# Optimization experiments

Hardware: AMD Instinct MI355X
Metric: run time of the kernel (lower is better)

Reference implementation:

```python
import jax, jax.numpy as jnp
import numpy as np

# module config (init_kwargs)
AH, AW = 14, 14            # aligned_height, aligned_width
SCALE = 0.25               # spatial_scale
RATIO = 2                  # sampling_ratio
SHIFT = 0.0                # spatial_shift (added in feature-map coords)
HALF_PART = 0              # 0 = full box
ROI_SCALE = 1.0            # box rescale about its center


def setup_inputs() -> dict:
    key = jax.random.key(0)
    kf, kb, kx, ky, kw, kh = jax.random.split(key, 6)
    B, C, H, W = 2, 256, 200, 272
    N = 256
    features = jax.random.normal(kf, (B, C, H, W), dtype=jnp.float32)
    img_h, img_w = H / SCALE, W / SCALE
    bidx = jax.random.randint(kb, (N,), 0, B).astype(jnp.float32)
    x1 = jax.random.uniform(kx, (N,)) * (img_w * 0.6)
    y1 = jax.random.uniform(ky, (N,)) * (img_h * 0.6)
    bw = 32.0 + jax.random.uniform(kw, (N,)) * (img_w * 0.35)
    bh = 32.0 + jax.random.uniform(kh, (N,)) * (img_h * 0.35)
    rois = jnp.stack([bidx, x1, y1, x1 + bw, y1 + bh], axis=1).astype(jnp.float32)
    return {"features": features, "rois": rois}


def _lin_idx(coord, size):
    # bilinear index/weight prep with RoIAlign boundary rules
    valid = (coord > -1.0) & (coord < float(size))
    c = jnp.clip(coord, 0.0, float(size - 1))
    lo = jnp.floor(c)
    hi = jnp.minimum(lo + 1.0, float(size - 1))
    frac = c - lo
    return lo.astype(jnp.int32), hi.astype(jnp.int32), frac, valid.astype(coord.dtype)


def _roi_mask_align(features, rois):
    B, C, H, W = features.shape
    N = rois.shape[0]
    PH, PW, r = AH + 1, AW + 1, RATIO
    b = rois[:, 0].astype(jnp.int32)
    # to feature-map coords, with roi_scale about the box center and spatial_shift
    x1, y1, x2, y2 = (rois[:, 1] * SCALE, rois[:, 2] * SCALE,
                      rois[:, 3] * SCALE, rois[:, 4] * SCALE)
    cx, cy = 0.5 * (x1 + x2), 0.5 * (y1 + y2)
    hw, hh = 0.5 * (x2 - x1) * ROI_SCALE, 0.5 * (y2 - y1) * ROI_SCALE
    x1, x2 = cx - hw + SHIFT, cx + hw + SHIFT
    y1, y2 = cy - hh + SHIFT, cy + hh + SHIFT
    roi_w = jnp.maximum(x2 - x1, 1.0)
    roi_h = jnp.maximum(y2 - y1, 1.0)
    bin_w = roi_w / PW
    bin_h = roi_h / PH
    # sample coords, separable: sx [N, PW*r], sy [N, PH*r]
    ix = jnp.arange(PW * r, dtype=jnp.float32)
    iy = jnp.arange(PH * r, dtype=jnp.float32)
    sx = x1[:, None] + (ix[None, :] + 0.5) * (bin_w[:, None] / r)
    sy = y1[:, None] + (iy[None, :] + 0.5) * (bin_h[:, None] / r)
    y_lo, y_hi, fy, vy = _lin_idx(sy, H)
    x_lo, x_hi, fx, vx = _lin_idx(sx, W)
    featsT = jnp.transpose(features, (0, 2, 3, 1))  # [B,H,W,C]
    bb = b[:, None, None]
    gather = lambda yi, xi: featsT[bb, yi[:, :, None], xi[:, None, :]]  # [N,Sy,Sx,C]
    wy0, wy1 = 1.0 - fy, fy
    wx0, wx1 = 1.0 - fx, fx
    val = (gather(y_lo, x_lo) * (wy0[:, :, None] * wx0[:, None, :])[..., None]
           + gather(y_lo, x_hi) * (wy0[:, :, None] * wx1[:, None, :])[..., None]
           + gather(y_hi, x_lo) * (wy1[:, :, None] * wx0[:, None, :])[..., None]
           + gather(y_hi, x_hi) * (wy1[:, :, None] * wx1[:, None, :])[..., None])
    val = val * (vy[:, :, None] * vx[:, None, :])[..., None]
    # average the r*r samples per bin -> [N, PH, PW, C]
    val = val.reshape(N, PH, r, PW, r, C).mean(axis=(2, 4))
    return jnp.transpose(val, (0, 3, 1, 2))  # [N, C, PH, PW]


def reference(features, rois):
    x = _roi_mask_align(features, rois)  # [N, C, AH+1, AW+1]
    # avg_pool2d(kernel=2, stride=1)
    out = 0.25 * (x[..., :-1, :-1] + x[..., 1:, :-1]
                  + x[..., :-1, 1:] + x[..., 1:, 1:])
    return out  # [N, C, AH, AW]
```

## Files before the change

kernel.cpp:

```cpp
#include <hip/hip_runtime.h>


#define AH_  14
#define AW_  14
#define C_   256
#define H_   200
#define W_   272
#define HW_  (H_ * W_)
#define CPB  4
#define WBUF 2056

#define GLOAD_LDS16(g, l)                                                     \
  __builtin_amdgcn_global_load_lds(                                           \
      (const __attribute__((address_space(1))) void*)(g),                     \
      (__attribute__((address_space(3))) void*)(l), 16, 0, 0)

__global__ __launch_bounds__(128)
void roi_mask_align_avg_kernel(const float* __restrict__ feat,
                               const float* __restrict__ rois,
                               float* __restrict__ out) {
    __shared__ float Ls[2][WBUF];

    const int p   = blockIdx.x;
    const int xcd = p & 7;
    const int q   = p >> 3;
    const int n   = q & 255;
    const int cgi = q >> 8;
    const int cg  = cgi * 8 + xcd;
    const int c0  = cg * CPB;

    const int tid  = threadIdx.x;
    const int wave = tid >> 6;
    const int lane = tid & 63;
    const int half = lane >> 5;
    const int ix   = lane & 31;

    float* __restrict__ LsW = Ls[wave];
    {
        float4* L4 = (float4*)LsW;
        for (int o = lane; o < WBUF / 4; o += 64)
            L4[o] = make_float4(0.f, 0.f, 0.f, 0.f);
    }
    asm volatile("s_waitcnt lgkmcnt(0)" ::: "memory");

    const float r0f = rois[n * 5 + 0];
    const float x1s = rois[n * 5 + 1] * 0.25f;
    const float y1s = rois[n * 5 + 2] * 0.25f;
    const float x2s = rois[n * 5 + 3] * 0.25f;
    const float y2s = rois[n * 5 + 4] * 0.25f;
    const int   b   = (int)r0f;

    const float cx = 0.5f * (x1s + x2s), cy = 0.5f * (y1s + y2s);
    const float hw = 0.5f * (x2s - x1s), hh = 0.5f * (y2s - y1s);
    const float x1 = cx - hw, x2 = cx + hw;
    const float y1 = cy - hh, y2 = cy + hh;
    const float roi_w = fmaxf(x2 - x1, 1.0f);
    const float roi_h = fmaxf(y2 - y1, 1.0f);
    const float sub_w = roi_w * (1.0f / 15.0f) * 0.5f;
    const float sub_h = roi_h * (1.0f / 15.0f) * 0.5f;

    const float sx  = x1 + ((float)ix + 0.5f) * sub_w;
    const bool  vx_ = (sx > -1.0f) && (sx < (float)W_) && (ix < 30);
    const float ccx = fminf(fmaxf(sx, 0.0f), (float)(W_ - 1));
    const float lox = floorf(ccx);
    const int   xl  = (int)lox;
    const int   xh  = min(xl + 1, W_ - 1);
    const float fx  = ccx - lox;
    const float vmx = vx_ ? 1.0f : 0.0f;
    const float wx0 = (1.0f - fx) * vmx;
    const float wx1 = fx * vmx;

    const int s0    = __builtin_amdgcn_readfirstlane(xl);
    const int s0c0  = min(s0, W_ - 128);
    const int s0c1  = max(min(s0 - 8, W_ - 128), 0);
    const int s0ch  = half ? s0c1 : s0c0;
    const int xh29  = __builtin_amdgcn_readlane(xh, 29);
    const int spanh = xh29 - s0ch;
    const bool ldact = (ix * 4) <= spanh;
    const int iA    = half * 128 + (xl - s0ch);

    const float* __restrict__ bpA = feat + ((size_t)b * C_ + c0) * (size_t)HW_;
    const float* __restrict__ gAl = bpA + (size_t)half * HW_ + s0ch + 4 * ix;
    const float* __restrict__ gBl = gAl + 2 * HW_;

    const int  aw   = ix >> 1;
    const bool emit = ((lane & 1) == 0) && (aw < AW_);
    const int  iy0  = wave * 14;

    auto geom = [&](int iy, int& olo, int& ohi, float& wy0, float& wy1) {
        const float sy  = y1 + ((float)iy + 0.5f) * sub_h;
        const bool  vy_ = (sy > -1.0f) && (sy < (float)H_);
        const float ccy = fminf(fmaxf(sy, 0.0f), (float)(H_ - 1));
        const float loy = floorf(ccy);
        const float fy  = ccy - loy;
        const float vmy = vy_ ? 1.0f : 0.0f;
        wy0 = (1.0f - fy) * vmy;
        wy1 = fy * vmy;
        const int yl_s = __builtin_amdgcn_readfirstlane((int)loy);
        const int yh_s = min(yl_s + 1, H_ - 1);
        olo = yl_s * W_;
        ohi = yh_s * W_;
    };
    auto stage = [&](int bb, int olo, int ohi) {
        float* d = LsW + bb * 1024;
        if (ldact) {
            GLOAD_LDS16(gAl + olo, d);
            GLOAD_LDS16(gBl + olo, d + 256);
            GLOAD_LDS16(gAl + ohi, d + 512);
            GLOAD_LDS16(gBl + ohi, d + 768);
        }
    };

    int   olo_c, ohi_c;  float wy0_c, wy1_c;
    geom(iy0, olo_c, ohi_c, wy0_c, wy1_c);
    stage(0, olo_c, ohi_c);

    float outA[7], outB[7];
    float prevSA = 0.f, prevSB = 0.f, PA = 0.f, PB = 0.f;

    #pragma unroll
    for (int i = 0; i < 16; ++i) {
        int olo_n, ohi_n; float wy0_n, wy1_n;
        geom(iy0 + i + 1, olo_n, ohi_n, wy0_n, wy1_n);

        asm volatile("s_waitcnt lgkmcnt(0)" ::: "memory");

        stage((i + 1) & 1, olo_n, ohi_n);

        asm volatile("s_waitcnt vmcnt(4)" ::: "memory");

        const float* d = LsW + (i & 1) * 1024;
        const float alo0 = d[iA],       alo1 = d[iA + 1];
        const float blo0 = d[256 + iA], blo1 = d[256 + iA + 1];
        const float ahi0 = d[512 + iA], ahi1 = d[512 + iA + 1];
        const float bhi0 = d[768 + iA], bhi1 = d[768 + iA + 1];

        const float w00 = wy0_c * wx0, w01 = wy0_c * wx1;
        const float w10 = wy1_c * wx0, w11 = wy1_c * wx1;
        PA += alo0 * w00 + alo1 * w01 + ahi0 * w10 + ahi1 * w11;
        PB += blo0 * w00 + blo1 * w01 + bhi0 * w10 + bhi1 * w11;

        if (i & 1) {
            const float tA = PA + __shfl_xor(PA, 1, 64);
            const float uA = tA + __shfl_down(tA, 2, 64);
            const float tB = PB + __shfl_xor(PB, 1, 64);
            const float uB = tB + __shfl_down(tB, 2, 64);
            const int kk = i >> 1;
            if (kk > 0) {
                outA[kk - 1] = (prevSA + uA) * 0.0625f;
                outB[kk - 1] = (prevSB + uB) * 0.0625f;
            }
            prevSA = uA; prevSB = uB;
            PA = 0.f; PB = 0.f;
        }
        olo_c = olo_n; ohi_c = ohi_n; wy0_c = wy0_n; wy1_c = wy1_n;
    }

    asm volatile("s_waitcnt vmcnt(0)" ::: "memory");
    if (emit) {
        #pragma unroll
        for (int k = 0; k < 7; ++k) {
            LsW[half * 98 + k * AW_ + aw]       = outA[k];
            LsW[(2 + half) * 98 + k * AW_ + aw] = outB[k];
        }
    }

    float* __restrict__ op = out + ((size_t)n * C_ + c0) * (AH_ * AW_);
    for (int o = lane; o < CPB * 7 * AW_; o += 64) {
        const int ch  = o / 98;
        const int rem = o - ch * 98;
        op[ch * (AH_ * AW_) + wave * 98 + rem] = LsW[o];
    }
}

extern "C" void kernel_launch(void* const* d_in, const int* in_sizes, int n_in,
                              void* d_out, int out_size, void* d_ws, size_t ws_size,
                              hipStream_t stream) {
    const float* feat = (const float*)d_in[0];
    const float* rois = (const float*)d_in[1];
    float* out = (float*)d_out;
    const int grid = 256 * (C_ / CPB);
    roi_mask_align_avg_kernel<<<grid, 128, 0, stream>>>(feat, rois, out);
}
```

Baseline: 252.7 us.

## Reuse loaded feature rows across consecutive y samples and drop double buffering

Precomputes per-sample y geometry once per lane and classifies each sample row as a full reuse, a shift (the previous hi row becomes lo), or a new load. Only rows that are actually new get fetched into LDS, which cuts redundant global loads when samples share rows. The LDS zero-init and the double buffer are removed, and the launch bound is raised to 8 blocks for higher occupancy. The trade-off is that each load is now waited on synchronously (vmcnt(0)), so the previous overlap of prefetch with compute is lost.

```diff
diff --git a/kernel.cpp b/kernel.cpp
--- a/kernel.cpp
+++ b/kernel.cpp
@@ -8,18 +8,17 @@
 #define W_   272
 #define HW_  (H_ * W_)
 #define CPB  4
-#define WBUF 2056
 
 #define GLOAD_LDS16(g, l)                                                     \
   __builtin_amdgcn_global_load_lds(                                           \
       (const __attribute__((address_space(1))) void*)(g),                     \
       (__attribute__((address_space(3))) void*)(l), 16, 0, 0)
 
-__global__ __launch_bounds__(128)
+__global__ __launch_bounds__(128, 8)
 void roi_mask_align_avg_kernel(const float* __restrict__ feat,
                                const float* __restrict__ rois,
                                float* __restrict__ out) {
-    __shared__ float Ls[2][WBUF];
+    __shared__ float Ls[2][1024];
 
     const int p   = blockIdx.x;
     const int xcd = p & 7;
@@ -36,12 +35,6 @@
     const int ix   = lane & 31;
 
     float* __restrict__ LsW = Ls[wave];
-    {
-        float4* L4 = (float4*)LsW;
-        for (int o = lane; o < WBUF / 4; o += 64)
-            L4[o] = make_float4(0.f, 0.f, 0.f, 0.f);
-    }
-    asm volatile("s_waitcnt lgkmcnt(0)" ::: "memory");
 
     const float r0f = rois[n * 5 + 0];
     const float x1s = rois[n * 5 + 1] * 0.25f;
@@ -71,72 +64,80 @@
     const float wx1 = fx * vmx;
 
     const int s0    = __builtin_amdgcn_readfirstlane(xl);
-    const int s0c0  = min(s0, W_ - 128);
-    const int s0c1  = max(min(s0 - 8, W_ - 128), 0);
-    const int s0ch  = half ? s0c1 : s0c0;
+    const int s0c   = min(s0, W_ - 128);
     const int xh29  = __builtin_amdgcn_readlane(xh, 29);
-    const int spanh = xh29 - s0ch;
+    const int spanh = xh29 - s0c;
     const bool ldact = (ix * 4) <= spanh;
-    const int iA    = half * 128 + (xl - s0ch);
+    const int iA    = half * 128 + (vx_ ? (xl - s0c) : 0);
 
     const float* __restrict__ bpA = feat + ((size_t)b * C_ + c0) * (size_t)HW_;
-    const float* __restrict__ gAl = bpA + (size_t)half * HW_ + s0ch + 4 * ix;
+    const float* __restrict__ gAl = bpA + (size_t)half * HW_ + s0c + 4 * ix;
     const float* __restrict__ gBl = gAl + 2 * HW_;
 
     const int  aw   = ix >> 1;
     const bool emit = ((lane & 1) == 0) && (aw < AW_);
     const int  iy0  = wave * 14;
 
-    auto geom = [&](int iy, int& olo, int& ohi, float& wy0, float& wy1) {
-        const float sy  = y1 + ((float)iy + 0.5f) * sub_h;
-        const bool  vy_ = (sy > -1.0f) && (sy < (float)H_);
-        const float ccy = fminf(fmaxf(sy, 0.0f), (float)(H_ - 1));
-        const float loy = floorf(ccy);
-        const float fy  = ccy - loy;
-        const float vmy = vy_ ? 1.0f : 0.0f;
-        wy0 = (1.0f - fy) * vmy;
-        wy1 = fy * vmy;
-        const int yl_s = __builtin_amdgcn_readfirstlane((int)loy);
-        const int yh_s = min(yl_s + 1, H_ - 1);
-        olo = yl_s * W_;
-        ohi = yh_s * W_;
-    };
-    auto stage = [&](int bb, int olo, int ohi) {
-        float* d = LsW + bb * 1024;
-        if (ldact) {
-            GLOAD_LDS16(gAl + olo, d);
-            GLOAD_LDS16(gBl + olo, d + 256);
-            GLOAD_LDS16(gAl + ohi, d + 512);
-            GLOAD_LDS16(gBl + ohi, d + 768);
-        }
-    };
+    const int   l    = lane & 15;
+    const float syl  = y1 + ((float)(iy0 + l) + 0.5f) * sub_h;
+    const bool  vyl  = (syl > -1.0f) && (syl < (float)H_);
+    const float ccyl = fminf(fmaxf(syl, 0.0f), (float)(H_ - 1));
+    const float loyl = floorf(ccyl);
+    const float fyl  = ccyl - loyl;
+    const float vmyl = vyl ? 1.0f : 0.0f;
+    const int   yll  = (int)loyl;
+    const int   yhl  = min(yll + 1, H_ - 1);
+    const int   wy0b = __float_as_int((1.0f - fyl) * vmyl);
+    const int   wy1b = __float_as_int(fyl * vmyl);
+    const int   olol = yll * W_;
+    const int   ohil = yhl * W_;
+    const int   pyll = __shfl_up(yll, 1, 64);
+    const int   pyhl = __shfl_up(yhl, 1, 64);
+    const int   casel = (l == 0) ? 2
+                       : (yll == pyll) ? 0
+                       : (yll == pyhl) ? 1 : 2;
 
-    int   olo_c, ohi_c;  float wy0_c, wy1_c;
-    geom(iy0, olo_c, ohi_c, wy0_c, wy1_c);
-    stage(0, olo_c, ohi_c);
-
+    float alo0 = 0.f, alo1 = 0.f, ahi0 = 0.f, ahi1 = 0.f;
+    float blo0 = 0.f, blo1 = 0.f, bhi0 = 0.f, bhi1 = 0.f;
     float outA[7], outB[7];
     float prevSA = 0.f, prevSB = 0.f, PA = 0.f, PB = 0.f;
 
     #pragma unroll
     for (int i = 0; i < 16; ++i) {
-        int olo_n, ohi_n; float wy0_n, wy1_n;
-        geom(iy0 + i + 1, olo_n, ohi_n, wy0_n, wy1_n);
+        const int   sc  = __builtin_amdgcn_readlane(casel, i);
+        const float wy0 = __int_as_float(__builtin_amdgcn_readlane(wy0b, i));
+        const float wy1 = __int_as_float(__builtin_amdgcn_readlane(wy1b, i));
 
-        asm volatile("s_waitcnt lgkmcnt(0)" ::: "memory");
+        if (sc == 1) {
+            alo0 = ahi0; alo1 = ahi1; blo0 = bhi0; blo1 = bhi1;
+            const int ohi = __builtin_amdgcn_readlane(ohil, i);
+            asm volatile("s_waitcnt lgkmcnt(0)" ::: "memory");
+            if (ldact) {
+                GLOAD_LDS16(gAl + ohi, LsW + 512);
+                GLOAD_LDS16(gBl + ohi, LsW + 768);
+            }
+            asm volatile("s_waitcnt vmcnt(0)" ::: "memory");
+            ahi0 = LsW[512 + iA]; ahi1 = LsW[512 + iA + 1];
+            bhi0 = LsW[768 + iA]; bhi1 = LsW[768 + iA + 1];
+        } else if (sc == 2) {
+            const int olo = __builtin_amdgcn_readlane(olol, i);
+            const int ohi = __builtin_amdgcn_readlane(ohil, i);
+            asm volatile("s_waitcnt lgkmcnt(0)" ::: "memory");
+            if (ldact) {
+                GLOAD_LDS16(gAl + olo, LsW);
+                GLOAD_LDS16(gBl + olo, LsW + 256);
+                GLOAD_LDS16(gAl + ohi, LsW + 512);
+                GLOAD_LDS16(gBl + ohi, LsW + 768);
+            }
+            asm volatile("s_waitcnt vmcnt(0)" ::: "memory");
+            alo0 = LsW[iA];       alo1 = LsW[iA + 1];
+            blo0 = LsW[256 + iA]; blo1 = LsW[256 + iA + 1];
+            ahi0 = LsW[512 + iA]; ahi1 = LsW[512 + iA + 1];
+            bhi0 = LsW[768 + iA]; bhi1 = LsW[768 + iA + 1];
+        }
 
-        stage((i + 1) & 1, olo_n, ohi_n);
-
-        asm volatile("s_waitcnt vmcnt(4)" ::: "memory");
-
-        const float* d = LsW + (i & 1) * 1024;
-        const float alo0 = d[iA],       alo1 = d[iA + 1];
-        const float blo0 = d[256 + iA], blo1 = d[256 + iA + 1];
-        const float ahi0 = d[512 + iA], ahi1 = d[512 + iA + 1];
-        const float bhi0 = d[768 + iA], bhi1 = d[768 + iA + 1];
-
-        const float w00 = wy0_c * wx0, w01 = wy0_c * wx1;
-        const float w10 = wy1_c * wx0, w11 = wy1_c * wx1;
+        const float w00 = wy0 * wx0, w01 = wy0 * wx1;
+        const float w10 = wy1 * wx0, w11 = wy1 * wx1;
         PA += alo0 * w00 + alo1 * w01 + ahi0 * w10 + ahi1 * w11;
         PB += blo0 * w00 + blo1 * w01 + bhi0 * w10 + bhi1 * w11;
 
@@ -153,10 +154,8 @@
             prevSA = uA; prevSB = uB;
             PA = 0.f; PB = 0.f;
         }
-        olo_c = olo_n; ohi_c = ohi_n; wy0_c = wy0_n; wy1_c = wy1_n;
     }
 
-    asm volatile("s_waitcnt vmcnt(0)" ::: "memory");
     if (emit) {
         #pragma unroll
         for (int k = 0; k < 7; ++k) {
@@ -164,7 +163,6 @@
             LsW[(2 + half) * 98 + k * AW_ + aw] = outB[k];
         }
     }
-
     float* __restrict__ op = out + ((size_t)n * C_ + c0) * (AH_ * AW_);
     for (int o = lane; o < CPB * 7 * AW_; o += 64) {
         const int ch  = o / 98;
```

Result: faster. 245.2 us (-3.0%).
